# Kernel optimization log

Hardware: AMD Instinct MI355X
Metric: run time of the kernel (lower is better)

The kernel has to match this reference:

```python
import jax, jax.numpy as jnp
import numpy as np

D_MODEL = 2048
B, L = 4, 2048


def _dwconv(x, w, b):
    # x: (B, D, L), w: (D, 1, 3), b: (D,). Causal depthwise conv (PyTorch pad=2 then [...,:L]).
    y = jax.lax.conv_general_dilated(
        x, w, window_strides=(1,), padding=[(2, 0)],
        feature_group_count=x.shape[1], dimension_numbers=("NCH", "OIH", "NCH"))
    return y + b[None, :, None]


def setup_inputs() -> dict:
    key = jax.random.key(0)
    ks = jax.random.split(key, 12)
    D = D_MODEL
    s = 0.02
    inp = {
        "u": jax.random.normal(ks[0], (B, L, D), jnp.float32),
        "Wq": jax.random.normal(ks[1], (D, D), jnp.float32) * s,
        "bq": jnp.zeros((D,), jnp.float32),
        "Wk": jax.random.normal(ks[2], (D, D), jnp.float32) * s,
        "bk": jnp.zeros((D,), jnp.float32),
        "Wv": jax.random.normal(ks[3], (D, D), jnp.float32) * s,
        "bv": jnp.zeros((D,), jnp.float32),
        "convq_w": jax.random.normal(ks[4], (D, 1, 3), jnp.float32) * 0.5,
        "convq_b": jnp.zeros((D,), jnp.float32),
        "convk_w": jax.random.normal(ks[5], (D, 1, 3), jnp.float32) * 0.5,
        "convk_b": jnp.zeros((D,), jnp.float32),
        "ssm_kernel": jax.random.normal(ks[6], (D, L), jnp.float32) * 0.01,  # H = d_model (head_dim=1)
        "D_skip": jax.random.normal(ks[7], (D,), jnp.float32),
        "Wo": jax.random.normal(ks[8], (D, D), jnp.float32) * s,
        "bo": jnp.zeros((D,), jnp.float32),
    }
    return inp


def reference(u, Wq, bq, Wk, bk, Wv, bv, convq_w, convq_b, convk_w, convk_b,
              ssm_kernel, D_skip, Wo, bo):
    # u: (B, L, H)  head_dim = 1 so H == d_model
    Lq = u.shape[1]
    fft_size = 2 * Lq  # L_kernel + L with l_max=None, rate=1

    # q/k/v projections (W @ u.T + b in torch == u @ W.T + b)
    q = jnp.einsum("blh,eh->ble", u, Wq) + bq
    k = jnp.einsum("blh,eh->ble", u, Wk) + bk
    v = jnp.einsum("blh,eh->ble", u, Wv) + bv
    q = jnp.transpose(q, (0, 2, 1))  # (B, H, L)
    k = jnp.transpose(k, (0, 2, 1))
    v = jnp.transpose(v, (0, 2, 1))

    # causal depthwise short convs
    q = _dwconv(q, convq_w, convq_b)
    k = _dwconv(k, convk_w, convk_b)

    # head_dim = 1: kv outer product collapses to elementwise product (B, H, L)
    kv = k * v

    # FFT long convolution: torch does rfft(kv)/n * rfft(kernel), irfft norm='forward'
    # which equals the standard unnormalized circular conv below.
    kv_f = jnp.fft.rfft(kv, n=fft_size)
    kernel_f = jnp.fft.rfft(ssm_kernel, n=fft_size)  # (H, F)
    y = jnp.fft.irfft(kv_f * kernel_f, n=fft_size)[..., :Lq]

    # D skip and q gating
    y = (y + kv * D_skip[None, :, None]) * q  # (B, H, L)

    # output projection
    y = jnp.transpose(y, (0, 2, 1))  # (B, L, H)
    return jnp.einsum("blh,eh->ble", y, Wo) + bo
```

## Files before the change

kernel.cpp:

```cpp
#include <hip/hip_runtime.h>
#include <cstdint>
#include <cstddef>

#define DD 2048
#define LL 2048
#define BB 4
#define MM (BB * LL)
#define NN 6144

typedef __bf16 bf16;
typedef __bf16 bf16x8 __attribute__((ext_vector_type(8)));
typedef __bf16 bf16x4 __attribute__((ext_vector_type(4)));
typedef __bf16 bf16x2 __attribute__((ext_vector_type(2)));
typedef float f32x4 __attribute__((ext_vector_type(4)));

__device__ __forceinline__ void gload16(const void* g, void* l) {
    __builtin_amdgcn_global_load_lds(
        (const __attribute__((address_space(1))) void*)g,
        (__attribute__((address_space(3))) void*)l, 16, 0, 0);
}

__global__ __launch_bounds__(256) void cvt_f32_bf16(const float* __restrict__ s,
                                                    bf16* __restrict__ d, int n8) {
    int i = blockIdx.x * 256 + threadIdx.x;
    if (i >= n8) return;
    const float4* sp = (const float4*)s + (size_t)i * 2;
    float4 a = sp[0], b = sp[1];
    bf16x8 o;
    o[0] = (bf16)a.x; o[1] = (bf16)a.y; o[2] = (bf16)a.z; o[3] = (bf16)a.w;
    o[4] = (bf16)b.x; o[5] = (bf16)b.y; o[6] = (bf16)b.z; o[7] = (bf16)b.w;
    *((bf16x8*)d + i) = o;
}

__device__ __forceinline__ void stage_half(const bf16* g, bf16* l, size_t rstep, int tid) {
    gload16(g, l + tid * 8);
    gload16(g + rstep, l + 4096 + tid * 8);
}

#define MFMA_BLK(IOFF)                                                          \
    __builtin_amdgcn_s_setprio(1);                                              \
    _Pragma("unroll") for (int j = 0; j < 4; j++)                               \
        _Pragma("unroll") for (int i = 0; i < 4; i++)                           \
            acc[(IOFF) + i][j] = __builtin_amdgcn_mfma_f32_16x16x32_bf16(       \
                af[i], bq[j], acc[(IOFF) + i][j], 0, 0, 0);                     \
    __builtin_amdgcn_s_setprio(0);

template <int NT>
__device__ __forceinline__ void mma256_loop(const bf16* gA, const bf16* gB,
                                            int Kdim, bf16* lds,
                                            f32x4 (&acc)[8][4]) {
    const int tid = threadIdx.x;
    const int wave = tid >> 6, lane = tid & 63;
    const int wm = wave >> 2, wn = wave & 3;
    const int fm = lane & 15, fg = lane >> 4;
    const size_t rstep = (size_t)128 * Kdim;
    const int koff = ((fg ^ ((fm >> 1) & 3)) << 3);
    const int aoff = (wm * 128 + fm) * 32 + koff;
    const int boff = (wn * 64 + fm) * 32 + koff;

    bf16* const A0 = lds;
    bf16* const B0 = lds + 32768;

#pragma unroll
    for (int i = 0; i < 8; i++)
#pragma unroll
        for (int j = 0; j < 4; j++) acc[i][j] = (f32x4){0.f, 0.f, 0.f, 0.f};

    stage_half(gA, A0, rstep, tid);
    stage_half(gB, B0, rstep, tid);
    stage_half(gA + 32, A0 + 8192, rstep, tid);
    stage_half(gB + 32, B0 + 8192, rstep, tid);

    bf16x8 af[4], bq[4];

    for (int t = 0; t < NT; ++t) {
        const int c = t & 1;
        bf16* const Ac = A0 + c * 16384;
        bf16* const Bc = B0 + c * 16384;
        bf16* const An = A0 + (c ^ 1) * 16384;
        bf16* const Bn = B0 + (c ^ 1) * 16384;
        const bf16* a1 = gA + (t + 1) * 64;
        const bf16* b1 = gB + (t + 1) * 64;
        const bool st = (t + 1 < NT);

        asm volatile("s_waitcnt vmcnt(4)" ::: "memory");
        __builtin_amdgcn_s_barrier();
#pragma unroll
        for (int i = 0; i < 4; i++) af[i] = *(const bf16x8*)(Ac + aoff + i * 512);
#pragma unroll
        for (int j = 0; j < 4; j++) bq[j] = *(const bf16x8*)(Bc + boff + j * 512);
        if (st) stage_half(a1, An, rstep, tid);
        __builtin_amdgcn_s_barrier();
        asm volatile("s_waitcnt lgkmcnt(0)" ::: "memory");
        MFMA_BLK(0)

        __builtin_amdgcn_s_barrier();
#pragma unroll
        for (int i = 0; i < 4; i++) af[i] = *(const bf16x8*)(Ac + aoff + (i + 4) * 512);
        if (st) stage_half(b1, Bn, rstep, tid);
        __builtin_amdgcn_s_barrier();
        asm volatile("s_waitcnt lgkmcnt(0)" ::: "memory");
        MFMA_BLK(4)

        if (st) { asm volatile("s_waitcnt vmcnt(4)" ::: "memory"); }
        else    { asm volatile("s_waitcnt vmcnt(0)" ::: "memory"); }
        __builtin_amdgcn_s_barrier();
#pragma unroll
        for (int i = 0; i < 4; i++) af[i] = *(const bf16x8*)(Ac + 8192 + aoff + i * 512);
#pragma unroll
        for (int j = 0; j < 4; j++) bq[j] = *(const bf16x8*)(Bc + 8192 + boff + j * 512);
        if (st) stage_half(a1 + 32, An + 8192, rstep, tid);
        __builtin_amdgcn_s_barrier();
        asm volatile("s_waitcnt lgkmcnt(0)" ::: "memory");
        MFMA_BLK(0)

        __builtin_amdgcn_s_barrier();
#pragma unroll
        for (int i = 0; i < 4; i++) af[i] = *(const bf16x8*)(Ac + 8192 + aoff + (i + 4) * 512);
        if (st) stage_half(b1 + 32, Bn + 8192, rstep, tid);
        __builtin_amdgcn_s_barrier();
        asm volatile("s_waitcnt lgkmcnt(0)" ::: "memory");
        MFMA_BLK(4)
    }
}

__global__ __launch_bounds__(512, 2) void gemm_qkv(const bf16* __restrict__ A,
                                                   const bf16* __restrict__ Bm,
                                                   const float* __restrict__ bqp,
                                                   const float* __restrict__ bkp,
                                                   const float* __restrict__ bvp,
                                                   bf16* __restrict__ CtOut) {
    __shared__ bf16 lds[65536];
    const int id = blockIdx.x;
    const int xcd = id & 7, li = id >> 3;
    const int m0 = (xcd * 4 + (li & 3)) << 8;
    const int n0 = (li >> 2) << 8;

    const int tid = threadIdx.x;
    const int wave = tid >> 6, lane = tid & 63;
    const int srow = tid >> 2;
    const int skx = (((lane & 3) ^ ((lane >> 3) & 3)) << 3);
    const bf16* gA = A + (size_t)(m0 + srow) * DD + skx;
    const bf16* gB = Bm + (size_t)(n0 + srow) * DD + skx;

    f32x4 acc[8][4];
    mma256_loop<DD / 64>(gA, gB, DD, lds, acc);

    __syncthreads();
    const int wm = wave >> 2, wn = wave & 3;
    const int fm = lane & 15, fg = lane >> 4;
    const float* bp = (n0 < 2048) ? bqp : ((n0 < 4096) ? bkp : bvp);
    const int nb = n0 & 2047;
#pragma unroll
    for (int j = 0; j < 4; j++) {
        const int col = wn * 64 + j * 16 + fm;
        const float bvv = bp[nb + col];
        const int csw = (col & 7) << 3;
#pragma unroll
        for (int i = 0; i < 8; i++) {
            const int row = (wm * 128 + i * 16 + fg * 4) ^ csw;
            bf16x4 o;
#pragma unroll
            for (int r = 0; r < 4; r++) o[r] = (bf16)(acc[i][j][r] + bvv);
            *(bf16x4*)&lds[col * 256 + row] = o;
        }
    }
    __syncthreads();
    const int ccol = tid >> 5, chunk = tid & 31;
#pragma unroll
    for (int p = 0; p < 16; p++) {
        const int col = p * 16 + ccol;
        bf16x8 vv = *(const bf16x8*)&lds[col * 256 + ((chunk * 8) ^ ((col & 7) << 3))];
        *(bf16x8*)(CtOut + (size_t)(n0 + col) * MM + m0 + chunk * 8) = vv;
    }
}

__global__ __launch_bounds__(512, 2) void gemm_bt_f32(const bf16* __restrict__ A,
                                                      const bf16* __restrict__ Bm,
                                                      const float* __restrict__ bias,
                                                      float* __restrict__ C,
                                                      int Ndim, int Kdim) {
    __shared__ bf16 lds[65536];
    const int id = blockIdx.x;
    const int xcd = id & 7, li = id >> 3;
    const int m0 = (xcd * 4 + (li & 3)) << 8;
    const int n0 = (li >> 2) << 8;

    const int tid = threadIdx.x;
    const int wave = tid >> 6, lane = tid & 63;
    const int srow = tid >> 2;
    const int skx = (((lane & 3) ^ ((lane >> 3) & 3)) << 3);
    const bf16* gA = A + (size_t)(m0 + srow) * Kdim + skx;
    const bf16* gB = Bm + (size_t)(n0 + srow) * Kdim + skx;

    f32x4 acc[8][4];
    mma256_loop<DD / 64>(gA, gB, Kdim, lds, acc);

    const int wm = wave >> 2, wn = wave & 3;
    const int fm = lane & 15, fg = lane >> 4;
#pragma unroll
    for (int j = 0; j < 4; j++) {
        const int col = n0 + wn * 64 + j * 16 + fm;
        const float bvv = bias[col];
#pragma unroll
        for (int i = 0; i < 8; i++) {
#pragma unroll
            for (int r = 0; r < 4; r++) {
                const int row = m0 + wm * 128 + i * 16 + fg * 4 + r;
                C[(size_t)row * Ndim + col] = acc[i][j][r] + bvv;
            }
        }
    }
}

__global__ __launch_bounds__(256) void dwconv_kv2(
    const bf16* __restrict__ qkvT,
    const float* __restrict__ cqw, const float* __restrict__ cqb,
    const float* __restrict__ ckw, const float* __restrict__ ckb,
    bf16* __restrict__ qcT, bf16* __restrict__ kvT) {
    const int bid = blockIdx.x;
    const int b = bid >> 11, d = bid & (DD - 1);
    const int tid = threadIdx.x;
    const int l = tid * 8;

    const bf16* qR = qkvT + (size_t)d * MM + b * LL;
    const bf16* kR = qkvT + (size_t)(2048 + d) * MM + b * LL;
    const bf16* vR = qkvT + (size_t)(4096 + d) * MM + b * LL;

    const float q0 = cqw[d * 3], q1 = cqw[d * 3 + 1], q2 = cqw[d * 3 + 2];
    const float k0 = ckw[d * 3], k1 = ckw[d * 3 + 1], k2 = ckw[d * 3 + 2];
    const float qb = cqb[d], kb = ckb[d];

    bf16x8 qx = *(const bf16x8*)(qR + l);
    bf16x8 kx = *(const bf16x8*)(kR + l);
    bf16x8 vx = *(const bf16x8*)(vR + l);

    float xq[10], xk[10];
    xq[0] = 0.f; xq[1] = 0.f; xk[0] = 0.f; xk[1] = 0.f;
    if (l >= 2) {
        bf16x2 qh = *(const bf16x2*)(qR + l - 2);
        bf16x2 kh = *(const bf16x2*)(kR + l - 2);
        xq[0] = (float)qh[0]; xq[1] = (float)qh[1];
        xk[0] = (float)kh[0]; xk[1] = (float)kh[1];
    }
#pragma unroll
    for (int c = 0; c < 8; c++) { xq[c + 2] = (float)qx[c]; xk[c + 2] = (float)kx[c]; }

    bf16x8 oq, okv;
#pragma unroll
    for (int c = 0; c < 8; c++) {
        float qc = q0 * xq[c] + q1 * xq[c + 1] + q2 * xq[c + 2] + qb;
        float kc = k0 * xk[c] + k1 * xk[c + 1] + k2 * xk[c + 2] + kb;
        oq[c] = (bf16)qc;
        okv[c] = (bf16)(kc * (float)vx[c]);
    }
    const size_t o = ((size_t)b * DD + d) * LL + l;
    *(bf16x8*)(qcT + o) = oq;
    *(bf16x8*)(kvT + o) = okv;
}

__global__ __launch_bounds__(128, 2) void longconv_gate(
    const bf16* __restrict__ kvT, const bf16* __restrict__ qcT,
    const float* __restrict__ kern, const float* __restrict__ Dskip,
    bf16* __restrict__ ygT) {
    __shared__ bf16 kv_ls[4 * 2112];
    __shared__ float krev_f[2112];
    const int d = blockIdx.x;
    const int tid = threadIdx.x;

    {
        const int bb = tid >> 5, t32 = tid & 31;
#pragma unroll
        for (int c = 0; c < 8; ++c) {
            const int l = (c * 32 + t32) * 8;
            bf16x8 v = *(const bf16x8*)(kvT + ((size_t)bb * DD + d) * LL + l);
            *(bf16x8*)&kv_ls[2112 * bb + 48 + l] = v;
        }
        if (tid < 48) {
#pragma unroll
            for (int b2 = 0; b2 < 4; b2++) kv_ls[2112 * b2 + tid] = (bf16)0.f;
        } else if (tid < 64) {
#pragma unroll
            for (int b2 = 0; b2 < 4; b2++) kv_ls[2112 * b2 + 2048 + tid] = (bf16)0.f;
        }
    }
    {
        const float* kr = kern + (size_t)d * LL;
#pragma unroll
        for (int c = 0; c < 16; ++c) {
            const int x = c * 128 + tid;
            krev_f[x] = kr[2047 - x];
        }
        if (tid < 64) krev_f[2048 + tid] = 0.f;
    }
    __syncthreads();

    const int lane = tid & 63;
    const int w = __builtin_amdgcn_readfirstlane(tid >> 6);
    const int n = lane & 15, q = lane >> 4;
    const int b = n & 3, pp = n >> 2;
    const int cB = 2112 * b + 16 * pp + 8 * q;

    f32x4 acc[16];
#pragma unroll
    for (int s = 0; s < 16; s++) acc[s] = (f32x4){0.f, 0.f, 0.f, 0.f};

    for (int it = 0; it < 64; ++it) {
        const int as = 2031 - 32 * it - n + 8 * q;
        float af[8];
#pragma unroll
        for (int j = 0; j < 8; j++) af[j] = krev_f[as + j];
        bf16x8 a;
#pragma unroll
        for (int j = 0; j < 8; j++) a[j] = (bf16)af[j];

        const int bbase = cB + 64 * w + 32 - 32 * it;
#pragma unroll
        for (int h = 0; h < 2; ++h) {
            bf16x8 bfr[8];
#pragma unroll
            for (int s8 = 0; s8 < 8; s8++) {
                const int s = h * 8 + s8;
                if (it <= 4 * s + 2 * w + 1)
                    bfr[s8] = *(const bf16x8*)&kv_ls[bbase + 128 * s];
            }
#pragma unroll
            for (int s8 = 0; s8 < 8; s8++) {
                const int s = h * 8 + s8;
                if (it <= 4 * s + 2 * w + 1)
                    acc[s] = __builtin_amdgcn_mfma_f32_16x16x32_bf16(
                        a, bfr[s8], acc[s], 0, 0, 0);
            }
        }
    }

    const float dsk = Dskip[d];
#pragma unroll
    for (int s = 0; s < 16; s++) {
        const int i = 2 * s + w;
        const int l = 64 * i + 16 * pp + 4 * q;
        const size_t gb = ((size_t)b * DD + d) * LL + l;
        bf16x4 qc4 = *(const bf16x4*)&qcT[gb];
        bf16x4 kv4 = *(const bf16x4*)&kv_ls[2112 * b + 48 + l];
        bf16x4 o;
#pragma unroll
        for (int r = 0; r < 4; r++) {
            float val = (acc[s][r] + (float)kv4[r] * dsk) * (float)qc4[r];
            o[r] = (bf16)val;
        }
        *(bf16x4*)&ygT[gb] = o;
    }
}

__global__ __launch_bounds__(256) void transpose_dl(const bf16* __restrict__ src,
                                                    bf16* __restrict__ dst) {
    __shared__ bf16 ts[64 * 64];
    const int b = blockIdx.z;
    const int l0 = blockIdx.x * 64, d0 = blockIdx.y * 64;
    const int tid = threadIdx.x;
    {
        const int r0 = tid >> 3, c8 = tid & 7;
#pragma unroll
        for (int h = 0; h < 2; h++) {
            const int r = r0 + h * 32;
            bf16x8 v = *(const bf16x8*)&src[((size_t)b * DD + d0 + r) * LL + l0 + c8 * 8];
            *(bf16x8*)&ts[r * 64 + ((c8 ^ (r & 7)) << 3)] = v;
        }
    }
    __syncthreads();
    const int l = tid & 63, dc0 = (tid >> 6) << 3;
#pragma unroll
    for (int half = 0; half < 2; half++) {
        const int dc = dc0 + half * 32;
        bf16x8 o;
#pragma unroll
        for (int j = 0; j < 8; j++) {
            const int r = dc + j;
            o[j] = ts[r * 64 + (((l >> 3) ^ (r & 7)) << 3) + (l & 7)];
        }
        *(bf16x8*)&dst[((size_t)b * LL + l0 + l) * DD + d0 + dc] = o;
    }
}

extern "C" void kernel_launch(void* const* d_in, const int* in_sizes, int n_in,
                              void* d_out, int out_size, void* d_ws, size_t ws_size,
                              hipStream_t stream) {
    const float* u   = (const float*)d_in[0];
    const float* Wq  = (const float*)d_in[1];
    const float* bq  = (const float*)d_in[2];
    const float* Wk  = (const float*)d_in[3];
    const float* bk  = (const float*)d_in[4];
    const float* Wv  = (const float*)d_in[5];
    const float* bv  = (const float*)d_in[6];
    const float* cqw = (const float*)d_in[7];
    const float* cqb = (const float*)d_in[8];
    const float* ckw = (const float*)d_in[9];
    const float* ckb = (const float*)d_in[10];
    const float* ssm = (const float*)d_in[11];
    const float* Dsk = (const float*)d_in[12];
    const float* Wo  = (const float*)d_in[13];
    const float* bo  = (const float*)d_in[14];

    char* w = (char*)d_ws;
    bf16* u_bf    = (bf16*)(w);
    bf16* Wqkv_bf = (bf16*)(w + 33554432ull);
    bf16* Wo_bf   = (bf16*)(w + 58720256ull);
    bf16* qkvT    = (bf16*)(w + 67108864ull);
    bf16* qcT     = (bf16*)(w + 167772160ull);
    bf16* kvT     = (bf16*)(w + 201326592ull);

    cvt_f32_bf16<<<8192, 256, 0, stream>>>(u, u_bf, MM * DD / 8);
    cvt_f32_bf16<<<2048, 256, 0, stream>>>(Wq, Wqkv_bf, DD * DD / 8);
    cvt_f32_bf16<<<2048, 256, 0, stream>>>(Wk, Wqkv_bf + 4194304, DD * DD / 8);
    cvt_f32_bf16<<<2048, 256, 0, stream>>>(Wv, Wqkv_bf + 8388608, DD * DD / 8);
    cvt_f32_bf16<<<2048, 256, 0, stream>>>(Wo, Wo_bf, DD * DD / 8);

    gemm_qkv<<<(MM / 256) * (NN / 256), 512, 0, stream>>>(u_bf, Wqkv_bf, bq, bk, bv, qkvT);

    dwconv_kv2<<<BB * DD, 256, 0, stream>>>(qkvT, cqw, cqb, ckw, ckb, qcT, kvT);

    bf16* ygT = u_bf;
    longconv_gate<<<DD, 128, 0, stream>>>(kvT, qcT, ssm, Dsk, ygT);

    bf16* ygTT = qkvT;
    dim3 gc(LL / 64, DD / 64, BB);
    transpose_dl<<<gc, 256, 0, stream>>>(ygT, ygTT);

    gemm_bt_f32<<<(MM / 256) * (DD / 256), 512, 0, stream>>>(ygTT, Wo_bf, bo,
                                                             (float*)d_out, DD, DD);
}
```

Baseline: 578.2 us.

## Merge conversion launches and restructure GEMM main loop with double-buffered fragments

Replaces five fp32-to-bf16 conversion launches with one kernel that picks its source by block index, removing launch overhead. The shared GEMM main loop now keeps two register sets of A and B fragments. It drops most of the per-subblock barriers and explicit lgkmcnt waits so LDS reads for the next MFMA block overlap the current one. This raises register pressure and relies on compiler-inserted waits and only two barriers per iteration being enough for correct LDS reuse, which risks races or spills.

```diff
diff --git a/kernel.cpp b/kernel.cpp
--- a/kernel.cpp
+++ b/kernel.cpp
@@ -20,10 +20,21 @@
         (__attribute__((address_space(3))) void*)l, 16, 0, 0);
 }
 
-__global__ __launch_bounds__(256) void cvt_f32_bf16(const float* __restrict__ s,
-                                                    bf16* __restrict__ d, int n8) {
-    int i = blockIdx.x * 256 + threadIdx.x;
-    if (i >= n8) return;
+__global__ __launch_bounds__(256) void cvt_all(
+    const float* __restrict__ u, const float* __restrict__ wq,
+    const float* __restrict__ wk, const float* __restrict__ wv,
+    const float* __restrict__ wo, bf16* __restrict__ u_bf,
+    bf16* __restrict__ wqkv, bf16* __restrict__ wo_bf) {
+    const int blk = blockIdx.x;
+    const float* s;
+    bf16* d;
+    int base;
+    if (blk < 8192)       { s = u;  d = u_bf;            base = 0; }
+    else if (blk < 10240) { s = wq; d = wqkv;            base = 8192; }
+    else if (blk < 12288) { s = wk; d = wqkv + 4194304;  base = 10240; }
+    else if (blk < 14336) { s = wv; d = wqkv + 8388608;  base = 12288; }
+    else                  { s = wo; d = wo_bf;           base = 14336; }
+    const int i = (blk - base) * 256 + threadIdx.x;
     const float4* sp = (const float4*)s + (size_t)i * 2;
     float4 a = sp[0], b = sp[1];
     bf16x8 o;
@@ -37,12 +48,12 @@
     gload16(g + rstep, l + 4096 + tid * 8);
 }
 
-#define MFMA_BLK(IOFF)                                                          \
+#define MFMA_BLK(AF, BQ, IOFF)                                                  \
     __builtin_amdgcn_s_setprio(1);                                              \
     _Pragma("unroll") for (int j = 0; j < 4; j++)                               \
         _Pragma("unroll") for (int i = 0; i < 4; i++)                           \
             acc[(IOFF) + i][j] = __builtin_amdgcn_mfma_f32_16x16x32_bf16(       \
-                af[i], bq[j], acc[(IOFF) + i][j], 0, 0, 0);                     \
+                AF[i], BQ[j], acc[(IOFF) + i][j], 0, 0, 0);                     \
     __builtin_amdgcn_s_setprio(0);
 
 template <int NT>
@@ -71,7 +82,7 @@
     stage_half(gA + 32, A0 + 8192, rstep, tid);
     stage_half(gB + 32, B0 + 8192, rstep, tid);
 
-    bf16x8 af[4], bq[4];
+    bf16x8 af0[4], af1[4], bq0[4], bq1[4];
 
     for (int t = 0; t < NT; ++t) {
         const int c = t & 1;
@@ -84,43 +95,31 @@
         const bool st = (t + 1 < NT);
 
         asm volatile("s_waitcnt vmcnt(4)" ::: "memory");
-        __builtin_amdgcn_s_barrier();
-#pragma unroll
-        for (int i = 0; i < 4; i++) af[i] = *(const bf16x8*)(Ac + aoff + i * 512);
-#pragma unroll
-        for (int j = 0; j < 4; j++) bq[j] = *(const bf16x8*)(Bc + boff + j * 512);
+        asm volatile("s_barrier" ::: "memory");
+#pragma unroll
+        for (int i = 0; i < 4; i++) af0[i] = *(const bf16x8*)(Ac + aoff + i * 512);
+#pragma unroll
+        for (int j = 0; j < 4; j++) bq0[j] = *(const bf16x8*)(Bc + boff + j * 512);
         if (st) stage_half(a1, An, rstep, tid);
-        __builtin_amdgcn_s_barrier();
-        asm volatile("s_waitcnt lgkmcnt(0)" ::: "memory");
-        MFMA_BLK(0)
-
-        __builtin_amdgcn_s_barrier();
-#pragma unroll
-        for (int i = 0; i < 4; i++) af[i] = *(const bf16x8*)(Ac + aoff + (i + 4) * 512);
+#pragma unroll
+        for (int i = 0; i < 4; i++) af1[i] = *(const bf16x8*)(Ac + aoff + (i + 4) * 512);
+        MFMA_BLK(af0, bq0, 0)
         if (st) stage_half(b1, Bn, rstep, tid);
-        __builtin_amdgcn_s_barrier();
-        asm volatile("s_waitcnt lgkmcnt(0)" ::: "memory");
-        MFMA_BLK(4)
 
         if (st) { asm volatile("s_waitcnt vmcnt(4)" ::: "memory"); }
         else    { asm volatile("s_waitcnt vmcnt(0)" ::: "memory"); }
-        __builtin_amdgcn_s_barrier();
-#pragma unroll
-        for (int i = 0; i < 4; i++) af[i] = *(const bf16x8*)(Ac + 8192 + aoff + i * 512);
-#pragma unroll
-        for (int j = 0; j < 4; j++) bq[j] = *(const bf16x8*)(Bc + 8192 + boff + j * 512);
+        asm volatile("s_barrier" ::: "memory");
+#pragma unroll
+        for (int i = 0; i < 4; i++) af0[i] = *(const bf16x8*)(Ac + 8192 + aoff + i * 512);
+#pragma unroll
+        for (int j = 0; j < 4; j++) bq1[j] = *(const bf16x8*)(Bc + 8192 + boff + j * 512);
         if (st) stage_half(a1 + 32, An + 8192, rstep, tid);
-        __builtin_amdgcn_s_barrier();
-        asm volatile("s_waitcnt lgkmcnt(0)" ::: "memory");
-        MFMA_BLK(0)
-
-        __builtin_amdgcn_s_barrier();
-#pragma unroll
-        for (int i = 0; i < 4; i++) af[i] = *(const bf16x8*)(Ac + 8192 + aoff + (i + 4) * 512);
+        MFMA_BLK(af1, bq0, 4)
+#pragma unroll
+        for (int i = 0; i < 4; i++) af1[i] = *(const bf16x8*)(Ac + 8192 + aoff + (i + 4) * 512);
         if (st) stage_half(b1 + 32, Bn + 8192, rstep, tid);
-        __builtin_amdgcn_s_barrier();
-        asm volatile("s_waitcnt lgkmcnt(0)" ::: "memory");
-        MFMA_BLK(4)
+        MFMA_BLK(af0, bq1, 0)
+        MFMA_BLK(af1, bq1, 4)
     }
 }
 
@@ -409,11 +408,7 @@
     bf16* qcT     = (bf16*)(w + 167772160ull);
     bf16* kvT     = (bf16*)(w + 201326592ull);
 
-    cvt_f32_bf16<<<8192, 256, 0, stream>>>(u, u_bf, MM * DD / 8);
-    cvt_f32_bf16<<<2048, 256, 0, stream>>>(Wq, Wqkv_bf, DD * DD / 8);
-    cvt_f32_bf16<<<2048, 256, 0, stream>>>(Wk, Wqkv_bf + 4194304, DD * DD / 8);
-    cvt_f32_bf16<<<2048, 256, 0, stream>>>(Wv, Wqkv_bf + 8388608, DD * DD / 8);
-    cvt_f32_bf16<<<2048, 256, 0, stream>>>(Wo, Wo_bf, DD * DD / 8);
+    cvt_all<<<16384, 256, 0, stream>>>(u, Wq, Wk, Wv, Wo, u_bf, Wqkv_bf, Wo_bf);
 
     gemm_qkv<<<(MM / 256) * (NN / 256), 512, 0, stream>>>(u_bf, Wqkv_bf, bq, bk, bv, qkvT);
 
```

Result: no change. 568.1 us (-1.7%).
